# Performance work log

Measured on AMD Instinct MI355X. Metric: run time of the kernel, lower is better.

The kernel has to match this reference:

```python
import jax, jax.numpy as jnp
import numpy as np
import math

B, S, D, H = 4, 2048, 1024, 16
HD = D // H  # head dim = 64


def _rope_tables(seq_len, dim, base=10000.0):
    half = dim // 2
    inv_freq = 1.0 / (base ** (jnp.arange(half, dtype=jnp.float32) / half))
    angles = jnp.arange(seq_len, dtype=jnp.float32)[:, None] * inv_freq[None, :]  # [S, half]
    return jnp.cos(angles), jnp.sin(angles)


def _apply_rope(x, cos, sin):
    # x: [B,H,S,HD]; half-split rotation (non-interleaved)
    half = x.shape[-1] // 2
    x1, x2 = x[..., :half], x[..., half:]
    c = cos[None, None, :, :]
    s = sin[None, None, :, :]
    return jnp.concatenate([x1 * c - x2 * s, x1 * s + x2 * c], axis=-1)


def setup_inputs() -> dict:
    key = jax.random.key(0)
    ks = jax.random.split(key, 7)
    sc = 1.0 / math.sqrt(D)
    return {
        "Q": jax.random.normal(ks[0], (B, S, D), jnp.float32),
        "K": jax.random.normal(ks[1], (B, S, D), jnp.float32),
        "V": jax.random.normal(ks[2], (B, S, D), jnp.float32),
        "Wq": jax.random.normal(ks[3], (D, D), jnp.float32) * sc,
        "bq": jnp.zeros((D,), jnp.float32),
        "Wk": jax.random.normal(ks[4], (D, D), jnp.float32) * sc,
        "bk": jnp.zeros((D,), jnp.float32),
        "Wv": jax.random.normal(ks[5], (D, D), jnp.float32) * sc,
        "bv": jnp.zeros((D,), jnp.float32),
        "Wo": jax.random.normal(ks[6], (D, D), jnp.float32) * sc,
        "bo": jnp.zeros((D,), jnp.float32),
    }


def reference(Q, K, V, Wq, bq, Wk, bk, Wv, bv, Wo, bo):
    bs, n, _ = Q.shape
    # projections (torch Linear: x @ W.T + b)
    q = (Q @ Wq.T + bq).reshape(bs, n, H, HD).transpose(0, 2, 1, 3)  # [B,H,S,HD]
    k = (K @ Wk.T + bk).reshape(bs, n, H, HD).transpose(0, 2, 1, 3)
    v = (V @ Wv.T + bv).reshape(bs, n, H, HD).transpose(0, 2, 1, 3)
    cos, sin = _rope_tables(n, HD)
    q = _apply_rope(q, cos, sin)
    k = _apply_rope(k, cos, sin)
    scores = jnp.einsum('bhqd,bhkd->bhqk', q, k) / math.sqrt(HD)
    causal = jnp.tril(jnp.ones((n, n), dtype=bool))
    scores = jnp.where(causal[None, None], scores, -jnp.inf)
    probs = jax.nn.softmax(scores, axis=-1)
    out = jnp.einsum('bhqk,bhkd->bhqd', probs, v)  # [B,H,S,HD]
    out = out.transpose(0, 2, 1, 3).reshape(bs, n, D)
    return out @ Wo.T + bo
```

## Files before the change

kernel.cpp:

```cpp
#include <hip/hip_runtime.h>
#include <hip/hip_bf16.h>

#define BB 4
#define SS 2048
#define DDIM 1024
#define HH 16
#define MTOT (BB*SS)

typedef __attribute__((ext_vector_type(8))) __bf16 bf16x8;
typedef __attribute__((ext_vector_type(4))) float f32x4;

static __device__ __forceinline__ unsigned short f2bf(float f) {
  union { float f; unsigned u; } v; v.f = f;
  unsigned r = v.u + 0x7FFFu + ((v.u >> 16) & 1u);
  return (unsigned short)(r >> 16);
}

static __device__ __forceinline__ bf16x8 ld_bf16x8(const void* p) {
  bf16x8 r;
  __builtin_memcpy(&r, p, 16);
  return r;
}

static __device__ __forceinline__ void gload_lds16(const void* g, void* l) {
  __builtin_amdgcn_global_load_lds(
      (const __attribute__((address_space(1))) unsigned int*)g,
      (__attribute__((address_space(3))) unsigned int*)l, 16, 0, 0);
}

__global__ void k_rope_tables(float* __restrict__ tc, float* __restrict__ ts) {
  int i = blockIdx.x * 256 + threadIdx.x;
  int s = i >> 5, d = i & 31;
  float inv = powf(10000.0f, -((float)d) / 32.0f);
  float a = (float)s * inv;
  tc[i] = cosf(a);
  ts[i] = sinf(a);
}

__global__ void k_cvt_bf16(const float* __restrict__ in,
                           unsigned short* __restrict__ out, int n4) {
  int i = blockIdx.x * 256 + threadIdx.x;
  if (i >= n4) return;
  float4 v = ((const float4*)in)[i];
  ushort4 o;
  o.x = f2bf(v.x); o.y = f2bf(v.y); o.z = f2bf(v.z); o.w = f2bf(v.w);
  ((ushort4*)out)[i] = o;
}

#define E_ROPE 0
#define E_VT   1
#define E_F32  2

template<int EPI>
__global__ __launch_bounds__(256, 2) void k_gemm(
    const unsigned short* __restrict__ A,
    const unsigned short* __restrict__ Bw,
    const float* __restrict__ bias,
    void* __restrict__ out,
    const float* __restrict__ tc, const float* __restrict__ ts,
    float scale)
{
  __shared__ unsigned short As[128*64];
  __shared__ unsigned short Bs[128*64];
  const int tid  = threadIdx.x;
  const int lane = tid & 63;
  const int wv   = tid >> 6;
  const int wr   = wv >> 1, wc = wv & 1;
  const int l15  = lane & 15, l4 = lane >> 4;
  const int bm0  = blockIdx.x * 128;
  const int bn0  = blockIdx.y * 128;

  const f32x4 fz = {0.f, 0.f, 0.f, 0.f};
  f32x4 acc[4][4];
#pragma unroll
  for (int m = 0; m < 4; ++m)
#pragma unroll
    for (int n = 0; n < 4; ++n) acc[m][n] = fz;

  const int srow = lane >> 3;
  const int scol = ((lane & 7) ^ srow) * 8;

  for (int kt = 0; kt < 16; ++kt) {
    const int k0 = kt * 64;
#pragma unroll
    for (int i = 0; i < 4; ++i) {
      const int c = wv * 4 + i;
      const int row = c * 8 + srow;
      gload_lds16(A  + (size_t)(bm0 + row) * 1024 + k0 + scol, (char*)As + c * 1024);
      gload_lds16(Bw + (size_t)(bn0 + row) * 1024 + k0 + scol, (char*)Bs + c * 1024);
    }
    __syncthreads();
#pragma unroll
    for (int h = 0; h < 2; ++h) {
      bf16x8 af[4], bfr[4];
#pragma unroll
      for (int m = 0; m < 4; ++m) {
        const int row = 64 * wr + 16 * m + l15;
        const int sl = ((l4 + 4 * h) ^ (l15 & 7)) * 8;
        af[m] = ld_bf16x8(&As[row * 64 + sl]);
      }
#pragma unroll
      for (int n = 0; n < 4; ++n) {
        const int row = 64 * wc + 16 * n + l15;
        const int sl = ((l4 + 4 * h) ^ (l15 & 7)) * 8;
        bfr[n] = ld_bf16x8(&Bs[row * 64 + sl]);
      }
#pragma unroll
      for (int m = 0; m < 4; ++m)
#pragma unroll
        for (int n = 0; n < 4; ++n)
          acc[m][n] = __builtin_amdgcn_mfma_f32_16x16x32_bf16(af[m], bfr[n], acc[m][n], 0, 0, 0);
    }
    __syncthreads();
  }

  if (EPI == E_ROPE) {
    unsigned short* O = (unsigned short*)out;
#pragma unroll
    for (int m = 0; m < 4; ++m) {
      const int row0 = bm0 + 64 * wr + 16 * m + 4 * l4;
#pragma unroll
      for (int n = 0; n < 2; ++n) {
        const int d = 16 * n + l15;
        const int col1 = bn0 + 64 * wc + d;
        const float b1 = bias[col1], b2 = bias[col1 + 32];
#pragma unroll
        for (int i = 0; i < 4; ++i) {
          const int row = row0 + i;
          const int s = row & (SS - 1);
          const float c = tc[s * 32 + d], sn = ts[s * 32 + d];
          const float x1 = acc[m][n][i] + b1;
          const float x2 = acc[m][n + 2][i] + b2;
          O[(size_t)row * 1024 + col1]      = f2bf((x1 * c - x2 * sn) * scale);
          O[(size_t)row * 1024 + col1 + 32] = f2bf((x1 * sn + x2 * c) * scale);
        }
      }
    }
  } else if (EPI == E_VT) {
    unsigned short* O = (unsigned short*)out;
    const int hh = (bn0 + 64 * wc) >> 6;
#pragma unroll
    for (int m = 0; m < 4; ++m) {
      const int row0 = bm0 + 64 * wr + 16 * m + 4 * l4;
      const int b_ = row0 >> 11;
      const int s0 = row0 & (SS - 1);
#pragma unroll
      for (int n = 0; n < 4; ++n) {
        const int d = 16 * n + l15;
        const float bb = bias[bn0 + 64 * wc + d];
        ushort4 o;
        o.x = f2bf(acc[m][n][0] + bb);
        o.y = f2bf(acc[m][n][1] + bb);
        o.z = f2bf(acc[m][n][2] + bb);
        o.w = f2bf(acc[m][n][3] + bb);
        *(ushort4*)&O[((size_t)(b_ * HH + hh) * 64 + d) * SS + s0] = o;
      }
    }
  } else {
    float* O = (float*)out;
#pragma unroll
    for (int m = 0; m < 4; ++m) {
      const int row0 = bm0 + 64 * wr + 16 * m + 4 * l4;
#pragma unroll
      for (int n = 0; n < 4; ++n) {
        const int col = bn0 + 64 * wc + 16 * n + l15;
        const float bb = bias[col];
#pragma unroll
        for (int i = 0; i < 4; ++i)
          O[(size_t)(row0 + i) * 1024 + col] = acc[m][n][i] + bb;
      }
    }
  }
}

__global__ __launch_bounds__(256, 4) void k_attn(
    const unsigned short* __restrict__ qr,
    const unsigned short* __restrict__ kr,
    const unsigned short* __restrict__ vT,
    unsigned short* __restrict__ ao)
{
  __shared__ unsigned short Ks[2][64*64];
  __shared__ unsigned short Vs[2][64*64];
  __shared__ unsigned short Ps[4][16*64];
  const int tid = threadIdx.x, lane = tid & 63, wv = tid >> 6;
  const int l15 = lane & 15, l4 = lane >> 4;
  const int pair = blockIdx.x & 15;
  const int bh = blockIdx.x >> 4;
  const int b_ = bh >> 4, h_ = bh & 15;

  const int srow = lane >> 3;
  const int scol = ((lane & 7) ^ srow) * 8;

  const f32x4 fz = {0.f, 0.f, 0.f, 0.f};

  for (int half = 0; half < 2; ++half) {
    const int j = half ? (31 - pair) : pair;
    const int q0 = j * 64;

    const size_t qoff = ((size_t)(b_ * SS + q0 + 16 * wv + l15)) * 1024 + h_ * 64 + l4 * 8;
    const bf16x8 aq0 = ld_bf16x8(&qr[qoff]);
    const bf16x8 aq1 = ld_bf16x8(&qr[qoff + 32]);

    f32x4 accO[4];
#pragma unroll
    for (int dt = 0; dt < 4; ++dt) accO[dt] = fz;
    float mrun[4], lrun[4];
#pragma unroll
    for (int i = 0; i < 4; ++i) { mrun[i] = -1e30f; lrun[i] = 0.f; }

    {
      const int k0 = 0;
#pragma unroll
      for (int i = 0; i < 2; ++i) {
        const int c = wv * 2 + i;
        const int row = c * 8 + srow;
        gload_lds16(kr + ((size_t)(b_ * SS + k0 + row)) * 1024 + h_ * 64 + scol,
                    (char*)&Ks[0][0] + c * 1024);
        gload_lds16(vT + ((size_t)(bh * 64 + row)) * SS + k0 + scol,
                    (char*)&Vs[0][0] + c * 1024);
      }
    }
    __syncthreads();

    int cur = 0;
    for (int kt = 0; kt <= j; ++kt) {
      if (kt < j) {
        const int k0 = (kt + 1) * 64;
        const int nb = cur ^ 1;
#pragma unroll
        for (int i = 0; i < 2; ++i) {
          const int c = wv * 2 + i;
          const int row = c * 8 + srow;
          gload_lds16(kr + ((size_t)(b_ * SS + k0 + row)) * 1024 + h_ * 64 + scol,
                      (char*)&Ks[nb][0] + c * 1024);
          gload_lds16(vT + ((size_t)(bh * 64 + row)) * SS + k0 + scol,
                      (char*)&Vs[nb][0] + c * 1024);
        }
      }

      const bool diag = (kt == j);
      f32x4 sc[4];
#pragma unroll
      for (int n = 0; n < 4; ++n) {
        if (!diag || n <= wv) {
          const int row = 16 * n + l15;
          const int sl0 = ((l4 + 0) ^ (l15 & 7)) * 8;
          const int sl1 = ((l4 + 4) ^ (l15 & 7)) * 8;
          bf16x8 kf0 = ld_bf16x8(&Ks[cur][row * 64 + sl0]);
          bf16x8 kf1 = ld_bf16x8(&Ks[cur][row * 64 + sl1]);
          sc[n] = __builtin_amdgcn_mfma_f32_16x16x32_bf16(aq0, kf0, fz, 0, 0, 0);
          sc[n] = __builtin_amdgcn_mfma_f32_16x16x32_bf16(aq1, kf1, sc[n], 0, 0, 0);
        } else {
          sc[n] = fz;
        }
      }
      if (diag) {
#pragma unroll
        for (int n = 0; n < 4; ++n)
#pragma unroll
          for (int i = 0; i < 4; ++i) {
            const int kj = 16 * n + l15;
            const int qi = 16 * wv + 4 * l4 + i;
            if (kj > qi) sc[n][i] = -1e30f;
          }
      }

      float tmax[4];
#pragma unroll
      for (int i = 0; i < 4; ++i) {
        float t = fmaxf(fmaxf(sc[0][i], sc[1][i]), fmaxf(sc[2][i], sc[3][i]));
        t = fmaxf(t, __shfl_xor(t, 1));
        t = fmaxf(t, __shfl_xor(t, 2));
        t = fmaxf(t, __shfl_xor(t, 4));
        t = fmaxf(t, __shfl_xor(t, 8));
        tmax[i] = t;
      }
      bool grow = (tmax[0] > mrun[0]) | (tmax[1] > mrun[1]) |
                  (tmax[2] > mrun[2]) | (tmax[3] > mrun[3]);
      if (__any(grow)) {
#pragma unroll
        for (int i = 0; i < 4; ++i) {
          const float mn = fmaxf(mrun[i], tmax[i]);
          const float alpha = exp2f(mrun[i] - mn);
          mrun[i] = mn;
          lrun[i] *= alpha;
#pragma unroll
          for (int dt = 0; dt < 4; ++dt) accO[dt][i] *= alpha;
        }
      }
      float pn[4][4];
#pragma unroll
      for (int i = 0; i < 4; ++i) {
        float rs = 0.f;
#pragma unroll
        for (int n = 0; n < 4; ++n) { pn[n][i] = exp2f(sc[n][i] - mrun[i]); rs += pn[n][i]; }
        rs += __shfl_xor(rs, 1);
        rs += __shfl_xor(rs, 2);
        rs += __shfl_xor(rs, 4);
        rs += __shfl_xor(rs, 8);
        lrun[i] += rs;
      }
#pragma unroll
      for (int n = 0; n < 4; ++n)
#pragma unroll
        for (int i = 0; i < 4; ++i) {
          const int r = 4 * l4 + i;
          const int cc = 16 * n + l15;
          const int phys = (cc >> 3) ^ (r & 7);
          Ps[wv][r * 64 + phys * 8 + (cc & 7)] = f2bf(pn[n][i]);
        }
#pragma unroll
      for (int kk = 0; kk < 2; ++kk) {
        if (diag && wv < 2 && kk == 1) continue;
        const int psl = ((l4 + 4 * kk) ^ (l15 & 7)) * 8;
        bf16x8 pa = ld_bf16x8(&Ps[wv][l15 * 64 + psl]);
#pragma unroll
        for (int dt = 0; dt < 4; ++dt) {
          const int row = 16 * dt + l15;
          const int vsl = ((l4 + 4 * kk) ^ (l15 & 7)) * 8;
          bf16x8 vb = ld_bf16x8(&Vs[cur][row * 64 + vsl]);
          accO[dt] = __builtin_amdgcn_mfma_f32_16x16x32_bf16(pa, vb, accO[dt], 0, 0, 0);
        }
      }
      __syncthreads();
      cur ^= 1;
    }

#pragma unroll
    for (int i = 0; i < 4; ++i) {
      const float inv = 1.0f / lrun[i];
      const size_t row = (size_t)(b_ * SS + q0 + 16 * wv + 4 * l4 + i);
#pragma unroll
      for (int dt = 0; dt < 4; ++dt)
        ao[row * 1024 + h_ * 64 + 16 * dt + l15] = f2bf(accO[dt][i] * inv);
    }
  }
}

extern "C" void kernel_launch(void* const* d_in, const int* in_sizes, int n_in,
                              void* d_out, int out_size, void* d_ws, size_t ws_size,
                              hipStream_t stream) {
  const float* Q  = (const float*)d_in[0];
  const float* K  = (const float*)d_in[1];
  const float* V  = (const float*)d_in[2];
  const float* Wq = (const float*)d_in[3];
  const float* bq = (const float*)d_in[4];
  const float* Wk = (const float*)d_in[5];
  const float* bk = (const float*)d_in[6];
  const float* Wv = (const float*)d_in[7];
  const float* bv = (const float*)d_in[8];
  const float* Wo = (const float*)d_in[9];
  const float* bo = (const float*)d_in[10];
  float* out = (float*)d_out;

  char* ws = (char*)d_ws;
  float* tc = (float*)(ws);
  float* ts = (float*)(ws + 256 * 1024);
  unsigned short* wqb = (unsigned short*)(ws + 512 * 1024);
  unsigned short* wkb = wqb + (1u << 20);
  unsigned short* wvb = wkb + (1u << 20);
  unsigned short* wob = wvb + (1u << 20);
  unsigned short* xb  = wob + (1u << 20);
  unsigned short* qrb = xb  + (size_t)MTOT * 1024;
  unsigned short* krb = qrb + (size_t)MTOT * 1024;
  unsigned short* vtb = krb + (size_t)MTOT * 1024;
  unsigned short* aob = vtb + (size_t)MTOT * 1024;

  k_rope_tables<<<256, 256, 0, stream>>>(tc, ts);
  k_cvt_bf16<<<1024, 256, 0, stream>>>(Wq, wqb, 1024 * 1024 / 4);
  k_cvt_bf16<<<1024, 256, 0, stream>>>(Wk, wkb, 1024 * 1024 / 4);
  k_cvt_bf16<<<1024, 256, 0, stream>>>(Wv, wvb, 1024 * 1024 / 4);
  k_cvt_bf16<<<1024, 256, 0, stream>>>(Wo, wob, 1024 * 1024 / 4);

  dim3 gg(MTOT / 128, 8);
  const float qsc = 0.125f * 1.4426950408889634f;

  k_cvt_bf16<<<MTOT * 1024 / 4 / 256, 256, 0, stream>>>(Q, xb, MTOT * 1024 / 4);
  k_gemm<E_ROPE><<<gg, 256, 0, stream>>>(xb, wqb, bq, qrb, tc, ts, qsc);
  k_cvt_bf16<<<MTOT * 1024 / 4 / 256, 256, 0, stream>>>(K, xb, MTOT * 1024 / 4);
  k_gemm<E_ROPE><<<gg, 256, 0, stream>>>(xb, wkb, bk, krb, tc, ts, 1.0f);
  k_cvt_bf16<<<MTOT * 1024 / 4 / 256, 256, 0, stream>>>(V, xb, MTOT * 1024 / 4);
  k_gemm<E_VT><<<gg, 256, 0, stream>>>(xb, wvb, bv, vtb, tc, ts, 1.0f);

  k_attn<<<64 * 16, 256, 0, stream>>>(qrb, krb, vtb, aob);

  k_gemm<E_F32><<<gg, 256, 0, stream>>>(aob, wob, bo, out, tc, ts, 1.0f);
}
```

Before: 390.2 us.

## Tune attention scheduling: lazy max rescale, MFMA priority, head-major blocks, packed RoPE table

Packs the RoPE cos/sin tables into one float2 array so each epilogue element needs a single load. Raises the GEMM occupancy hint from 2 to 3 blocks per CU. In attention, the block index now runs head-fastest so concurrent blocks cover different heads, and s_setprio is raised around the MFMA sections. The online softmax now rescales only when the new max exceeds the running max by more than 11 (log2 units), which skips many rescales but allows unnormalized exponentials up to 2^11 that fp32 and bf16 P must absorb.

```diff
diff --git a/kernel.cpp b/kernel.cpp
--- a/kernel.cpp
+++ b/kernel.cpp
@@ -28,13 +28,12 @@
       (__attribute__((address_space(3))) unsigned int*)l, 16, 0, 0);
 }
 
-__global__ void k_rope_tables(float* __restrict__ tc, float* __restrict__ ts) {
+__global__ void k_rope_tables(float2* __restrict__ t) {
   int i = blockIdx.x * 256 + threadIdx.x;
   int s = i >> 5, d = i & 31;
   float inv = powf(10000.0f, -((float)d) / 32.0f);
   float a = (float)s * inv;
-  tc[i] = cosf(a);
-  ts[i] = sinf(a);
+  t[i] = make_float2(cosf(a), sinf(a));
 }
 
 __global__ void k_cvt_bf16(const float* __restrict__ in,
@@ -52,12 +51,12 @@
 #define E_F32  2
 
 template<int EPI>
-__global__ __launch_bounds__(256, 2) void k_gemm(
+__global__ __launch_bounds__(256, 3) void k_gemm(
     const unsigned short* __restrict__ A,
     const unsigned short* __restrict__ Bw,
     const float* __restrict__ bias,
     void* __restrict__ out,
-    const float* __restrict__ tc, const float* __restrict__ ts,
+    const float2* __restrict__ tcs,
     float scale)
 {
   __shared__ unsigned short As[128*64];
@@ -128,11 +127,11 @@
         for (int i = 0; i < 4; ++i) {
           const int row = row0 + i;
           const int s = row & (SS - 1);
-          const float c = tc[s * 32 + d], sn = ts[s * 32 + d];
+          const float2 cs = tcs[s * 32 + d];
           const float x1 = acc[m][n][i] + b1;
           const float x2 = acc[m][n + 2][i] + b2;
-          O[(size_t)row * 1024 + col1]      = f2bf((x1 * c - x2 * sn) * scale);
-          O[(size_t)row * 1024 + col1 + 32] = f2bf((x1 * sn + x2 * c) * scale);
+          O[(size_t)row * 1024 + col1]      = f2bf((x1 * cs.x - x2 * cs.y) * scale);
+          O[(size_t)row * 1024 + col1 + 32] = f2bf((x1 * cs.y + x2 * cs.x) * scale);
         }
       }
     }
@@ -184,8 +183,8 @@
   __shared__ unsigned short Ps[4][16*64];
   const int tid = threadIdx.x, lane = tid & 63, wv = tid >> 6;
   const int l15 = lane & 15, l4 = lane >> 4;
-  const int pair = blockIdx.x & 15;
-  const int bh = blockIdx.x >> 4;
+  const int bh = blockIdx.x & 63;
+  const int pair = blockIdx.x >> 6;
   const int b_ = bh >> 4, h_ = bh & 15;
 
   const int srow = lane >> 3;
@@ -209,14 +208,13 @@
     for (int i = 0; i < 4; ++i) { mrun[i] = -1e30f; lrun[i] = 0.f; }
 
     {
-      const int k0 = 0;
 #pragma unroll
       for (int i = 0; i < 2; ++i) {
         const int c = wv * 2 + i;
         const int row = c * 8 + srow;
-        gload_lds16(kr + ((size_t)(b_ * SS + k0 + row)) * 1024 + h_ * 64 + scol,
+        gload_lds16(kr + ((size_t)(b_ * SS + row)) * 1024 + h_ * 64 + scol,
                     (char*)&Ks[0][0] + c * 1024);
-        gload_lds16(vT + ((size_t)(bh * 64 + row)) * SS + k0 + scol,
+        gload_lds16(vT + ((size_t)(bh * 64 + row)) * SS + scol,
                     (char*)&Vs[0][0] + c * 1024);
       }
     }
@@ -240,6 +238,7 @@
 
       const bool diag = (kt == j);
       f32x4 sc[4];
+      __builtin_amdgcn_s_setprio(1);
 #pragma unroll
       for (int n = 0; n < 4; ++n) {
         if (!diag || n <= wv) {
@@ -254,6 +253,7 @@
           sc[n] = fz;
         }
       }
+      __builtin_amdgcn_s_setprio(0);
       if (diag) {
 #pragma unroll
         for (int n = 0; n < 4; ++n)
@@ -268,16 +268,16 @@
       float tmax[4];
 #pragma unroll
       for (int i = 0; i < 4; ++i) {
-        float t = fmaxf(fmaxf(sc[0][i], sc[1][i]), fmaxf(sc[2][i], sc[3][i]));
+        float t = fmaxf(fmaxf(fmaxf(sc[0][i], sc[1][i]), sc[2][i]), sc[3][i]);
         t = fmaxf(t, __shfl_xor(t, 1));
         t = fmaxf(t, __shfl_xor(t, 2));
         t = fmaxf(t, __shfl_xor(t, 4));
         t = fmaxf(t, __shfl_xor(t, 8));
         tmax[i] = t;
       }
-      bool grow = (tmax[0] > mrun[0]) | (tmax[1] > mrun[1]) |
-                  (tmax[2] > mrun[2]) | (tmax[3] > mrun[3]);
-      if (__any(grow)) {
+      bool need = (tmax[0] > mrun[0] + 11.f) | (tmax[1] > mrun[1] + 11.f) |
+                  (tmax[2] > mrun[2] + 11.f) | (tmax[3] > mrun[3] + 11.f);
+      if (__any(need)) {
 #pragma unroll
         for (int i = 0; i < 4; ++i) {
           const float mn = fmaxf(mrun[i], tmax[i]);
@@ -309,6 +309,7 @@
           const int phys = (cc >> 3) ^ (r & 7);
           Ps[wv][r * 64 + phys * 8 + (cc & 7)] = f2bf(pn[n][i]);
         }
+      __builtin_amdgcn_s_setprio(1);
 #pragma unroll
       for (int kk = 0; kk < 2; ++kk) {
         if (diag && wv < 2 && kk == 1) continue;
@@ -322,6 +323,7 @@
           accO[dt] = __builtin_amdgcn_mfma_f32_16x16x32_bf16(pa, vb, accO[dt], 0, 0, 0);
         }
       }
+      __builtin_amdgcn_s_setprio(0);
       __syncthreads();
       cur ^= 1;
     }
@@ -354,8 +356,7 @@
   float* out = (float*)d_out;
 
   char* ws = (char*)d_ws;
-  float* tc = (float*)(ws);
-  float* ts = (float*)(ws + 256 * 1024);
+  float2* tcs = (float2*)(ws);
   unsigned short* wqb = (unsigned short*)(ws + 512 * 1024);
   unsigned short* wkb = wqb + (1u << 20);
   unsigned short* wvb = wkb + (1u << 20);
@@ -366,7 +367,7 @@
   unsigned short* vtb = krb + (size_t)MTOT * 1024;
   unsigned short* aob = vtb + (size_t)MTOT * 1024;
 
-  k_rope_tables<<<256, 256, 0, stream>>>(tc, ts);
+  k_rope_tables<<<256, 256, 0, stream>>>(tcs);
   k_cvt_bf16<<<1024, 256, 0, stream>>>(Wq, wqb, 1024 * 1024 / 4);
   k_cvt_bf16<<<1024, 256, 0, stream>>>(Wk, wkb, 1024 * 1024 / 4);
   k_cvt_bf16<<<1024, 256, 0, stream>>>(Wv, wvb, 1024 * 1024 / 4);
@@ -376,13 +377,13 @@
   const float qsc = 0.125f * 1.4426950408889634f;
 
   k_cvt_bf16<<<MTOT * 1024 / 4 / 256, 256, 0, stream>>>(Q, xb, MTOT * 1024 / 4);
-  k_gemm<E_ROPE><<<gg, 256, 0, stream>>>(xb, wqb, bq, qrb, tc, ts, qsc);
+  k_gemm<E_ROPE><<<gg, 256, 0, stream>>>(xb, wqb, bq, qrb, tcs, qsc);
   k_cvt_bf16<<<MTOT * 1024 / 4 / 256, 256, 0, stream>>>(K, xb, MTOT * 1024 / 4);
-  k_gemm<E_ROPE><<<gg, 256, 0, stream>>>(xb, wkb, bk, krb, tc, ts, 1.0f);
+  k_gemm<E_ROPE><<<gg, 256, 0, stream>>>(xb, wkb, bk, krb, tcs, 1.0f);
   k_cvt_bf16<<<MTOT * 1024 / 4 / 256, 256, 0, stream>>>(V, xb, MTOT * 1024 / 4);
-  k_gemm<E_VT><<<gg, 256, 0, stream>>>(xb, wvb, bv, vtb, tc, ts, 1.0f);
+  k_gemm<E_VT><<<gg, 256, 0, stream>>>(xb, wvb, bv, vtb, tcs, 1.0f);
 
   k_attn<<<64 * 16, 256, 0, stream>>>(qrb, krb, vtb, aob);
 
-  k_gemm<E_F32><<<gg, 256, 0, stream>>>(aob, wob, bo, out, tc, ts, 1.0f);
-}
+  k_gemm<E_F32><<<gg, 256, 0, stream>>>(aob, wob, bo, out, tcs, 1.0f);
+}
```

Result: faster. 378.7 us (-2.9%).
